# Optimization experiments

Measured on AMD Instinct MI355X. Metric: run time of the kernel, lower is better.

## Reference

```python
import jax, jax.numpy as jnp
import numpy as np

B, S, E = 4, 2048, 1024
H, HD, R = 16, 64, 32  # heads, head_dim, rank


def setup_inputs() -> dict:
    key = jax.random.key(0)
    ks = jax.random.split(key, 9)
    sc = 0.02
    return {
        "hidden_states": jax.random.normal(ks[0], (B, S, E), jnp.float32),
        "q_weight": jax.random.normal(ks[1], (E, E), jnp.float32) * sc,
        "q_bias": jax.random.normal(ks[2], (E,), jnp.float32) * sc,
        "k_weight": jax.random.normal(ks[3], (E, E), jnp.float32) * sc,
        "k_bias": jax.random.normal(ks[4], (E,), jnp.float32) * sc,
        "low_rank_value_weight": jax.random.normal(ks[5], (E, H * R), jnp.float32) * sc,
        "low_rank_value_bias": jax.random.normal(ks[6], (H * R,), jnp.float32) * sc,
        "low_rank_output_weight": jax.random.normal(ks[7], (H * R, E), jnp.float32) * sc,
        "output_bias": jax.random.normal(ks[8], (E,), jnp.float32) * sc,
    }


def reference(hidden_states, q_weight, q_bias, k_weight, k_bias,
              low_rank_value_weight, low_rank_value_bias,
              low_rank_output_weight, output_bias):
    b, s, _ = hidden_states.shape
    q = hidden_states @ q_weight + q_bias                       # [B,S,E]
    k = hidden_states @ k_weight + k_bias                       # [B,S,E]
    v = hidden_states @ low_rank_value_weight + low_rank_value_bias  # [B,S,H*R]
    q = q.reshape(b, s, H, HD).transpose(0, 2, 1, 3)            # [B,H,S,HD]
    k = k.reshape(b, s, H, HD).transpose(0, 2, 1, 3)
    v = v.reshape(b, s, H, R).transpose(0, 2, 1, 3)             # [B,H,S,R]
    scores = jnp.einsum('bhqd,bhkd->bhqk', q, k) / jnp.sqrt(jnp.float32(HD))
    causal = jnp.tril(jnp.ones((s, s), dtype=bool))
    scores = jnp.where(causal, scores, jnp.finfo(scores.dtype).min)
    probs = jax.nn.softmax(scores, axis=-1)                     # [B,H,S,S]
    attn = jnp.einsum('bhqk,bhkr->bhqr', probs, v)              # [B,H,S,R]
    attn = attn.transpose(0, 2, 1, 3).reshape(b, s, H * R)      # [B,S,H*R]
    out = attn @ low_rank_output_weight + output_bias           # [B,S,E]
    return out
```

## Files before the change

### kernel.cpp

```cpp
#include <hip/hip_runtime.h>

typedef _Float16 f16;
typedef __attribute__((ext_vector_type(4))) float f4;
typedef __attribute__((ext_vector_type(4))) _Float16 h4;
typedef __attribute__((ext_vector_type(8))) _Float16 h8;
typedef __attribute__((ext_vector_type(4))) float f32x4;
typedef __attribute__((ext_vector_type(4))) unsigned int u4;

#define SWZ(row, colByte) (((row) << 7) + ((colByte) ^ (((row) & 7) << 4)))

__global__ __launch_bounds__(256) void transpose_cast(
    const float* __restrict__ in, f16* __restrict__ out, int R, int C) {
  __shared__ float tile[32][33];
  const int t = threadIdx.x, tx = t & 31, ty = t >> 5;
  const int bc = blockIdx.x * 32, br = blockIdx.y * 32;
#pragma unroll
  for (int i = 0; i < 4; ++i)
    tile[ty + i * 8][tx] = in[(size_t)(br + ty + i * 8) * C + bc + tx];
  __syncthreads();
#pragma unroll
  for (int i = 0; i < 4; ++i)
    out[(size_t)(bc + ty + i * 8) * R + br + tx] = (f16)tile[tx][ty + i * 8];
}

__global__ __launch_bounds__(256) void hgemm_qkv(
    const float* __restrict__ A, const f16* __restrict__ Bt,
    const float* __restrict__ qb, const float* __restrict__ kb,
    const float* __restrict__ vb,
    f16* __restrict__ qf, f16* __restrict__ kf, f16* __restrict__ vf) {
  __shared__ f16 As[128 * 40];
  __shared__ f16 Bs[128 * 40];
  const int K = 1024;
  const int t = threadIdx.x;
  const int lane = t & 63, wave = t >> 6;
  const int wr = wave >> 1, wc = wave & 1;
  const int lrow = lane & 15, lk = lane >> 4;
  const int bm = blockIdx.y * 128;
  const int bnT = blockIdx.x;
  const int bn = bnT * 128;

  f32x4 acc[4][4];
#pragma unroll
  for (int i = 0; i < 4; ++i)
#pragma unroll
    for (int j = 0; j < 4; ++j) acc[i][j] = (f32x4)0.f;

  for (int kt = 0; kt < K; kt += 32) {
    {
      const int row = t >> 1, part = t & 1;
      const float* src = A + (size_t)(bm + row) * K + kt + part * 16;
      const f4 v0 = *(const f4*)(src + 0);
      const f4 v1 = *(const f4*)(src + 4);
      const f4 v2 = *(const f4*)(src + 8);
      const f4 v3 = *(const f4*)(src + 12);
      h8 lo, hi;
      lo[0] = (f16)v0.x; lo[1] = (f16)v0.y; lo[2] = (f16)v0.z; lo[3] = (f16)v0.w;
      lo[4] = (f16)v1.x; lo[5] = (f16)v1.y; lo[6] = (f16)v1.z; lo[7] = (f16)v1.w;
      hi[0] = (f16)v2.x; hi[1] = (f16)v2.y; hi[2] = (f16)v2.z; hi[3] = (f16)v2.w;
      hi[4] = (f16)v3.x; hi[5] = (f16)v3.y; hi[6] = (f16)v3.z; hi[7] = (f16)v3.w;
      *(h8*)&As[row * 40 + part * 16] = lo;
      *(h8*)&As[row * 40 + part * 16 + 8] = hi;
    }
#pragma unroll
    for (int i = 0; i < 2; ++i) {
      const int ch = t + i * 256;
      const int row = ch >> 2, part = ch & 3;
      *(u4*)&Bs[row * 40 + part * 8] =
          *(const u4*)(Bt + (size_t)(bn + row) * K + kt + part * 8);
    }
    __syncthreads();
    h8 af[4], bf[4];
#pragma unroll
    for (int f = 0; f < 4; ++f) {
      af[f] = *(const h8*)&As[(wr * 64 + f * 16 + lrow) * 40 + lk * 8];
      bf[f] = *(const h8*)&Bs[(wc * 64 + f * 16 + lrow) * 40 + lk * 8];
    }
#pragma unroll
    for (int i = 0; i < 4; ++i)
#pragma unroll
      for (int j = 0; j < 4; ++j)
        acc[i][j] = __builtin_amdgcn_mfma_f32_16x16x32_f16(af[i], bf[j], acc[i][j], 0, 0, 0);
    __syncthreads();
  }

  const float* bias;
  f16* outp;
  int nbase;
  if (bnT < 8) { bias = qb; outp = qf; nbase = 0; }
  else if (bnT < 16) { bias = kb; outp = kf; nbase = 1024; }
  else { bias = vb; outp = vf; nbase = 2048; }

#pragma unroll
  for (int fi = 0; fi < 4; ++fi) {
#pragma unroll
    for (int j = 0; j < 4; ++j) {
      const int grow = bm + wr * 64 + fi * 16 + lk * 4 + j;
      const int bb = grow >> 11, ss = grow & 2047;
#pragma unroll
      for (int fj = 0; fj < 4; ++fj) {
        const int gcol = bn + wc * 64 + fj * 16 + lrow;
        const int nl = gcol - nbase;
        const float g = acc[fi][fj][j] + bias[nl];
        if (bnT < 16) {
          outp[((size_t)(bb * 16 + (nl >> 6)) * 2048 + ss) * 64 + (nl & 63)] = (f16)g;
        } else {
          outp[((size_t)(bb * 16 + (nl >> 5)) * 2048 + ss) * 32 + (nl & 31)] = (f16)g;
        }
      }
    }
  }
}

__global__ __launch_bounds__(256) void hgemm_out(
    const f16* __restrict__ A, const f16* __restrict__ Bt,
    const float* __restrict__ bias, float* __restrict__ outp,
    const int N, const int K) {
  __shared__ f16 As[128 * 40];
  __shared__ f16 Bs[128 * 40];
  const int t = threadIdx.x;
  const int lane = t & 63, wave = t >> 6;
  const int wr = wave >> 1, wc = wave & 1;
  const int lrow = lane & 15, lk = lane >> 4;
  const int bm = blockIdx.y * 128, bn = blockIdx.x * 128;

  f32x4 acc[4][4];
#pragma unroll
  for (int i = 0; i < 4; ++i)
#pragma unroll
    for (int j = 0; j < 4; ++j) acc[i][j] = (f32x4)0.f;

  for (int kt = 0; kt < K; kt += 32) {
#pragma unroll
    for (int i = 0; i < 2; ++i) {
      const int ch = t + i * 256;
      const int row = ch >> 2, part = ch & 3;
      *(u4*)&As[row * 40 + part * 8] =
          *(const u4*)(A + (size_t)(bm + row) * K + kt + part * 8);
      *(u4*)&Bs[row * 40 + part * 8] =
          *(const u4*)(Bt + (size_t)(bn + row) * K + kt + part * 8);
    }
    __syncthreads();
    h8 af[4], bf[4];
#pragma unroll
    for (int f = 0; f < 4; ++f) {
      af[f] = *(const h8*)&As[(wr * 64 + f * 16 + lrow) * 40 + lk * 8];
      bf[f] = *(const h8*)&Bs[(wc * 64 + f * 16 + lrow) * 40 + lk * 8];
    }
#pragma unroll
    for (int i = 0; i < 4; ++i)
#pragma unroll
      for (int j = 0; j < 4; ++j)
        acc[i][j] = __builtin_amdgcn_mfma_f32_16x16x32_f16(af[i], bf[j], acc[i][j], 0, 0, 0);
    __syncthreads();
  }

#pragma unroll
  for (int fi = 0; fi < 4; ++fi) {
#pragma unroll
    for (int j = 0; j < 4; ++j) {
      const int grow = bm + wr * 64 + fi * 16 + lk * 4 + j;
#pragma unroll
      for (int fj = 0; fj < 4; ++fj) {
        const int gcol = bn + wc * 64 + fj * 16 + lrow;
        outp[(size_t)grow * N + gcol] = acc[fi][fj][j] + bias[gcol];
      }
    }
  }
}

__global__ __launch_bounds__(256) void attn_mfma(
    const f16* __restrict__ qf, const f16* __restrict__ kf,
    const f16* __restrict__ vf, f16* __restrict__ attf) {
  __shared__ f16 Ks[64 * 64];
  __shared__ f16 VsT[32 * 64];
  __shared__ f16 Ps[4 * 32 * 64];
  const int id = blockIdx.x;
  const int bh = id & 63;
  const int qblk = 15 - (id >> 6);
  const int qbase = qblk * 128;
  const int t = threadIdx.x;
  const int lane = t & 63, w = t >> 6;
  const int l15 = lane & 15, g = lane >> 4;
  const size_t kvbase = (size_t)bh * 2048;
  char* Pw = (char*)&Ps[w * 32 * 64];

  h8 qreg[2][2];
#pragma unroll
  for (int fj = 0; fj < 2; ++fj) {
    const int q = qbase + fj * 64 + w * 16 + l15;
#pragma unroll
    for (int ks = 0; ks < 2; ++ks) {
      h8 raw = *(const h8*)(qf + (kvbase + q) * 64 + ks * 32 + g * 8);
#pragma unroll
      for (int e = 0; e < 8; ++e) raw[e] = raw[e] * (f16)0.125f;
      qreg[fj][ks] = raw;
    }
  }

  f32x4 accO[2][2];
#pragma unroll
  for (int i = 0; i < 2; ++i)
#pragma unroll
    for (int j = 0; j < 2; ++j) accO[i][j] = (f32x4)0.f;
  float m2[2] = {-1.0e30f, -1.0e30f};
  float lsum[2] = {0.f, 0.f};

  const int ntiles = qblk * 2 + 2;
  for (int kt = 0; kt < ntiles; ++kt) {
    const int kbase = kt * 64;
    __syncthreads();
#pragma unroll
    for (int i = 0; i < 2; ++i) {
      const int idx = t + i * 256;
      const int row = idx >> 3, ch = idx & 7;
      *(u4*)((char*)Ks + SWZ(row, ch * 16)) =
          *(const u4*)(kf + (kvbase + kbase + row) * 64 + ch * 8);
    }
    {
      const int key = t >> 2, ch = t & 3;
      const u4 wv = *(const u4*)(vf + (kvbase + kbase + key) * 32 + ch * 8);
      const h8 hv = __builtin_bit_cast(h8, wv);
#pragma unroll
      for (int e = 0; e < 8; ++e) {
        const int row = ch * 8 + e;
        *(f16*)((char*)VsT + SWZ(row, key * 2)) = hv[e];
      }
    }
    __syncthreads();

    f32x4 accS[4][2];
#pragma unroll
    for (int i = 0; i < 4; ++i)
#pragma unroll
      for (int j = 0; j < 2; ++j) accS[i][j] = (f32x4)0.f;
#pragma unroll
    for (int ks = 0; ks < 2; ++ks) {
#pragma unroll
      for (int fim = 0; fim < 4; ++fim) {
        const h8 af = *(const h8*)((char*)Ks + SWZ(fim * 16 + l15, ks * 64 + g * 16));
#pragma unroll
        for (int fj = 0; fj < 2; ++fj)
          accS[fim][fj] = __builtin_amdgcn_mfma_f32_16x16x32_f16(af, qreg[fj][ks], accS[fim][fj], 0, 0, 0);
      }
    }

#pragma unroll
    for (int fj = 0; fj < 2; ++fj) {
      const int qg = qbase + fj * 64 + w * 16 + l15;
      const bool need_mask = (kbase + 63 > qbase + fj * 64 + w * 16);
      float sc[4][4];
      float mc = -1.0e30f;
#pragma unroll
      for (int fim = 0; fim < 4; ++fim)
#pragma unroll
        for (int j = 0; j < 4; ++j) {
          float v = accS[fim][fj][j];
          if (need_mask) {
            const int key = kbase + fim * 16 + g * 4 + j;
            v = (key <= qg) ? v : -1.0e30f;
          }
          sc[fim][j] = v;
          mc = fmaxf(mc, v);
        }
      mc = fmaxf(mc, __shfl_xor(mc, 16));
      mc = fmaxf(mc, __shfl_xor(mc, 32));
      if (!__all(mc <= m2[fj] + 1.5f)) {
        const float mnew = fmaxf(m2[fj], mc);
        const float corr = __expf(m2[fj] - mnew);
        m2[fj] = mnew;
        lsum[fj] *= corr;
#pragma unroll
        for (int j = 0; j < 4; ++j) {
          const float c = __shfl(corr, g * 4 + j);
          accO[fj][0][j] *= c;
          accO[fj][1][j] *= c;
        }
      }
      const float mloc = m2[fj];
      float ls = lsum[fj];
#pragma unroll
      for (int fim = 0; fim < 4; ++fim) {
        h4 hp;
#pragma unroll
        for (int j = 0; j < 4; ++j) {
          const float p = __expf(sc[fim][j] - mloc);
          ls += p;
          hp[j] = (f16)p;
        }
        *(h4*)(Pw + SWZ(fj * 16 + l15, fim * 32 + g * 8)) = hp;
      }
      lsum[fj] = ls;
    }

#pragma unroll
    for (int ks = 0; ks < 2; ++ks) {
      const h8 pa0 = *(const h8*)(Pw + SWZ(l15, ks * 64 + g * 16));
      const h8 pa1 = *(const h8*)(Pw + SWZ(16 + l15, ks * 64 + g * 16));
#pragma unroll
      for (int fr = 0; fr < 2; ++fr) {
        const h8 vb = *(const h8*)((char*)VsT + SWZ(fr * 16 + l15, ks * 64 + g * 16));
        accO[0][fr] = __builtin_amdgcn_mfma_f32_16x16x32_f16(pa0, vb, accO[0][fr], 0, 0, 0);
        accO[1][fr] = __builtin_amdgcn_mfma_f32_16x16x32_f16(pa1, vb, accO[1][fr], 0, 0, 0);
      }
    }
  }

  float inv[2];
#pragma unroll
  for (int fj = 0; fj < 2; ++fj) {
    float ls = lsum[fj];
    ls += __shfl_xor(ls, 16);
    ls += __shfl_xor(ls, 32);
    inv[fj] = 1.f / ls;
  }
  const int b = bh >> 4, h = bh & 15;
#pragma unroll
  for (int fo = 0; fo < 2; ++fo) {
#pragma unroll
    for (int j = 0; j < 4; ++j) {
      const float iv = __shfl(inv[fo], g * 4 + j);
      const int q = qbase + fo * 64 + w * 16 + g * 4 + j;
#pragma unroll
      for (int fr = 0; fr < 2; ++fr) {
        const int r = fr * 16 + l15;
        attf[((size_t)b * 2048 + q) * 512 + h * 32 + r] = (f16)(accO[fo][fr][j] * iv);
      }
    }
  }
}

extern "C" void kernel_launch(void* const* d_in, const int* in_sizes, int n_in,
                              void* d_out, int out_size, void* d_ws, size_t ws_size,
                              hipStream_t stream) {
  const float* hs = (const float*)d_in[0];
  const float* qw = (const float*)d_in[1];
  const float* qb = (const float*)d_in[2];
  const float* kw = (const float*)d_in[3];
  const float* kb = (const float*)d_in[4];
  const float* vw = (const float*)d_in[5];
  const float* vb = (const float*)d_in[6];
  const float* ow = (const float*)d_in[7];
  const float* ob = (const float*)d_in[8];
  float* out = (float*)d_out;
  char* ws = (char*)d_ws;

  f16* qf = (f16*)(ws);
  f16* kf = (f16*)(ws + ((size_t)16 << 20));
  f16* vf = (f16*)(ws + ((size_t)32 << 20));
  f16* attf = (f16*)(ws + ((size_t)40 << 20));
  f16* wqkv = (f16*)(ws + ((size_t)48 << 20));
  f16* owt = (f16*)(ws + ((size_t)54 << 20));

  transpose_cast<<<dim3(32, 32), 256, 0, stream>>>(qw, wqkv, 1024, 1024);
  transpose_cast<<<dim3(32, 32), 256, 0, stream>>>(kw, wqkv + (size_t)1024 * 1024, 1024, 1024);
  transpose_cast<<<dim3(16, 32), 256, 0, stream>>>(vw, wqkv + (size_t)2048 * 1024, 1024, 512);
  transpose_cast<<<dim3(32, 16), 256, 0, stream>>>(ow, owt, 512, 1024);

  hgemm_qkv<<<dim3(20, 64), 256, 0, stream>>>(hs, wqkv, qb, kb, vb, qf, kf, vf);
  attn_mfma<<<dim3(1024), 256, 0, stream>>>(qf, kf, vf, attf);
  hgemm_out<<<dim3(8, 64), 256, 0, stream>>>(attf, owt, ob, out, 1024, 512);
}
```

Before: 191.1 us.

## Pre-cast hidden states to fp16 and remap GEMM block order for XCD locality

```diff
diff --git a/kernel.cpp b/kernel.cpp
--- a/kernel.cpp
+++ b/kernel.cpp
@@ -9,6 +9,16 @@
 
 #define SWZ(row, colByte) (((row) << 7) + ((colByte) ^ (((row) & 7) << 4)))
 
+__global__ __launch_bounds__(256) void cast_f16(
+    const float* __restrict__ in, f16* __restrict__ out, int n4) {
+  for (int i = blockIdx.x * 256 + threadIdx.x; i < n4; i += gridDim.x * 256) {
+    const f4 v = ((const f4*)in)[i];
+    h4 h;
+    h.x = (f16)v.x; h.y = (f16)v.y; h.z = (f16)v.z; h.w = (f16)v.w;
+    ((h4*)out)[i] = h;
+  }
+}
+
 __global__ __launch_bounds__(256) void transpose_cast(
     const float* __restrict__ in, f16* __restrict__ out, int R, int C) {
   __shared__ float tile[32][33];
@@ -24,20 +34,22 @@
 }
 
 __global__ __launch_bounds__(256) void hgemm_qkv(
-    const float* __restrict__ A, const f16* __restrict__ Bt,
+    const f16* __restrict__ A, const f16* __restrict__ Bt,
     const float* __restrict__ qb, const float* __restrict__ kb,
     const float* __restrict__ vb,
     f16* __restrict__ qf, f16* __restrict__ kf, f16* __restrict__ vf) {
   __shared__ f16 As[128 * 40];
   __shared__ f16 Bs[128 * 40];
   const int K = 1024;
+  const int id = blockIdx.x;
+  const int swz = (id & 7) * 160 + (id >> 3);
+  const int bnT = swz % 20;
+  const int bm = (swz / 20) * 128;
+  const int bn = bnT * 128;
   const int t = threadIdx.x;
   const int lane = t & 63, wave = t >> 6;
   const int wr = wave >> 1, wc = wave & 1;
   const int lrow = lane & 15, lk = lane >> 4;
-  const int bm = blockIdx.y * 128;
-  const int bnT = blockIdx.x;
-  const int bn = bnT * 128;
 
   f32x4 acc[4][4];
 #pragma unroll
@@ -46,25 +58,12 @@
     for (int j = 0; j < 4; ++j) acc[i][j] = (f32x4)0.f;
 
   for (int kt = 0; kt < K; kt += 32) {
-    {
-      const int row = t >> 1, part = t & 1;
-      const float* src = A + (size_t)(bm + row) * K + kt + part * 16;
-      const f4 v0 = *(const f4*)(src + 0);
-      const f4 v1 = *(const f4*)(src + 4);
-      const f4 v2 = *(const f4*)(src + 8);
-      const f4 v3 = *(const f4*)(src + 12);
-      h8 lo, hi;
-      lo[0] = (f16)v0.x; lo[1] = (f16)v0.y; lo[2] = (f16)v0.z; lo[3] = (f16)v0.w;
-      lo[4] = (f16)v1.x; lo[5] = (f16)v1.y; lo[6] = (f16)v1.z; lo[7] = (f16)v1.w;
-      hi[0] = (f16)v2.x; hi[1] = (f16)v2.y; hi[2] = (f16)v2.z; hi[3] = (f16)v2.w;
-      hi[4] = (f16)v3.x; hi[5] = (f16)v3.y; hi[6] = (f16)v3.z; hi[7] = (f16)v3.w;
-      *(h8*)&As[row * 40 + part * 16] = lo;
-      *(h8*)&As[row * 40 + part * 16 + 8] = hi;
-    }
 #pragma unroll
     for (int i = 0; i < 2; ++i) {
       const int ch = t + i * 256;
       const int row = ch >> 2, part = ch & 3;
+      *(u4*)&As[row * 40 + part * 8] =
+          *(const u4*)(A + (size_t)(bm + row) * K + kt + part * 8);
       *(u4*)&Bs[row * 40 + part * 8] =
           *(const u4*)(Bt + (size_t)(bn + row) * K + kt + part * 8);
     }
@@ -117,11 +116,14 @@
     const int N, const int K) {
   __shared__ f16 As[128 * 40];
   __shared__ f16 Bs[128 * 40];
+  const int id = blockIdx.x;
+  const int swz = (id & 7) * 64 + (id >> 3);
+  const int bn = (swz & 7) * 128;
+  const int bm = (swz >> 3) * 128;
   const int t = threadIdx.x;
   const int lane = t & 63, wave = t >> 6;
   const int wr = wave >> 1, wc = wave & 1;
   const int lrow = lane & 15, lk = lane >> 4;
-  const int bm = blockIdx.y * 128, bn = blockIdx.x * 128;
 
   f32x4 acc[4][4];
 #pragma unroll
@@ -350,13 +352,15 @@
   f16* attf = (f16*)(ws + ((size_t)40 << 20));
   f16* wqkv = (f16*)(ws + ((size_t)48 << 20));
   f16* owt = (f16*)(ws + ((size_t)54 << 20));
-
+  f16* hsf = (f16*)(ws + ((size_t)56 << 20));
+
+  cast_f16<<<2048, 256, 0, stream>>>(hs, hsf, 8192 * 1024 / 4);
   transpose_cast<<<dim3(32, 32), 256, 0, stream>>>(qw, wqkv, 1024, 1024);
   transpose_cast<<<dim3(32, 32), 256, 0, stream>>>(kw, wqkv + (size_t)1024 * 1024, 1024, 1024);
   transpose_cast<<<dim3(16, 32), 256, 0, stream>>>(vw, wqkv + (size_t)2048 * 1024, 1024, 512);
   transpose_cast<<<dim3(32, 16), 256, 0, stream>>>(ow, owt, 512, 1024);
 
-  hgemm_qkv<<<dim3(20, 64), 256, 0, stream>>>(hs, wqkv, qb, kb, vb, qf, kf, vf);
+  hgemm_qkv<<<dim3(1280), 256, 0, stream>>>(hsf, wqkv, qb, kb, vb, qf, kf, vf);
   attn_mfma<<<dim3(1024), 256, 0, stream>>>(qf, kf, vf, attf);
-  hgemm_out<<<dim3(8, 64), 256, 0, stream>>>(attf, owt, ob, out, 1024, 512);
-}
+  hgemm_out<<<dim3(512), 256, 0, stream>>>(attf, owt, ob, out, 1024, 512);
+}
```

Result: faster. 176.9 us (-7.4%).
